# Kernel optimization log

Hardware: AMD Instinct MI355X
Metric: run time of the kernel (lower is better)

The kernel has to match this reference:

```python
import jax, jax.numpy as jnp
import numpy as np

B, S, D, H = 2, 2048, 1024, 16
DK = D // H  # 64
THETA = 10000.0


def setup_inputs() -> dict:
    key = jax.random.key(0)
    ks = jax.random.split(key, 5)
    std = float(np.sqrt(2.0 / (D + D)))
    x = jax.random.normal(ks[0], (B, S, D), dtype=jnp.float32)
    q_proj = jax.random.normal(ks[1], (D, D), dtype=jnp.float32) * std
    k_proj = jax.random.normal(ks[2], (D, D), dtype=jnp.float32) * std
    v_proj = jax.random.normal(ks[3], (D, D), dtype=jnp.float32) * std
    o_proj = jax.random.normal(ks[4], (D, D), dtype=jnp.float32) * std
    token_positions = jnp.arange(S, dtype=jnp.int32).reshape(1, S)
    return {"x": x, "token_positions": token_positions,
            "q_proj": q_proj, "k_proj": k_proj, "v_proj": v_proj, "o_proj": o_proj}


def _rope(t, pos):
    # t: [B, H, S, DK]; pos: [S]. Equivalent to multiplying by the block-diagonal
    # rotation matrix R[pos] in the source (interleaved 2x2 rotations).
    inv_freq = 1.0 / (THETA ** (2.0 * jnp.arange(DK // 2, dtype=jnp.float32) / DK))
    ang = pos.astype(jnp.float32)[:, None] * inv_freq[None, :]  # [S, DK/2]
    c, s = jnp.cos(ang), jnp.sin(ang)
    t0, t1 = t[..., 0::2], t[..., 1::2]
    out0 = c * t0 - s * t1
    out1 = s * t0 + c * t1
    return jnp.stack([out0, out1], axis=-1).reshape(t.shape)


def reference(x, token_positions, q_proj, k_proj, v_proj, o_proj):
    def split_heads(t):  # [B,S,D] -> [B,H,S,DK]
        return t.reshape(B, S, H, DK).transpose(0, 2, 1, 3)

    q = split_heads(jnp.einsum('bsd,ed->bse', x, q_proj))
    k = split_heads(jnp.einsum('bsd,ed->bse', x, k_proj))
    v = split_heads(jnp.einsum('bsd,ed->bse', x, v_proj))

    pos = token_positions[0]
    q = _rope(q, pos)
    k = _rope(k, pos)

    scores = jnp.einsum('bhqd,bhkd->bhqk', q, k) / jnp.sqrt(jnp.float32(DK))
    causal = jnp.tril(jnp.ones((S, S), dtype=bool))
    scores = jnp.where(causal, scores, -jnp.inf)

    # Faithful to source softmax: subtract the GLOBAL max (x.max()), then row-normalize.
    p = jnp.exp(scores - jnp.max(scores))
    p = p / jnp.sum(p, axis=-1, keepdims=True)

    attn = jnp.einsum('bhqk,bhkd->bhqd', p, v)
    attn = attn.transpose(0, 2, 1, 3).reshape(B, S, D)  # merge heads
    return jnp.einsum('bsd,ed->bse', attn, o_proj)
```

## Files before the change

### kernel.cpp

```cpp
#include <hip/hip_runtime.h>
#include <math.h>

#define B_  2
#define S_  2048
#define D_  1024
#define H_  16
#define DK_ 64
#define M_  (B_ * S_)

using u16 = unsigned short;
using u32 = unsigned int;
typedef __attribute__((ext_vector_type(8))) short  short8;
typedef __attribute__((ext_vector_type(4))) short  short4v;
typedef __attribute__((ext_vector_type(4))) float  float4v;
typedef __attribute__((ext_vector_type(4))) float  f32x4;
typedef __attribute__((ext_vector_type(4))) u32    u32x4;

__device__ __forceinline__ float bf2f(u16 h) {
  u32 u = ((u32)h) << 16;
  return __builtin_bit_cast(float, u);
}
__device__ __forceinline__ u16 f2bf(float f) {
  u32 u = __builtin_bit_cast(u32, f);
  u32 r = u + 0x7fffu + ((u >> 16) & 1u);
  return (u16)(r >> 16);
}

__device__ __forceinline__ void async16(const void* g, void* l) {
  __builtin_amdgcn_global_load_lds((const __attribute__((address_space(1))) void*)g,
                                   (__attribute__((address_space(3))) void*)l,
                                   16, 0, 0);
}

#define MFMA16(a, b, c) __builtin_amdgcn_mfma_f32_16x16x32_bf16((a), (b), (c), 0, 0, 0)

#define XG_  (M_ * D_ / 4)
#define WG_  (D_ * D_ / 4)
#define TOT_ (XG_ + 4 * WG_)
__global__ __launch_bounds__(256) void cvt5_kernel(
    const float* __restrict__ x,  const float* __restrict__ wq,
    const float* __restrict__ wk, const float* __restrict__ wv,
    const float* __restrict__ wo, u16* __restrict__ Xb, u16* __restrict__ Wqb,
    u16* __restrict__ Wkb, u16* __restrict__ Wvb, u16* __restrict__ Wob,
    float* __restrict__ tab, const void* __restrict__ posv) {
  int i = blockIdx.x * 256 + threadIdx.x;
  if (i >= TOT_) {
    const int j  = i - TOT_;
    const int s  = j >> 5, ii = j & 31;
    const int* p32 = (const int*)posv;
    const bool is64 = (p32[1] == 0 && p32[2] == 1);
    const int  ps   = is64 ? p32[2 * s] : p32[s];
    const float freq = exp2f(-0.4152410118609203f * (float)ii);
    float sn, cs;
    sincosf((float)ps * freq, &sn, &cs);
    tab[(size_t)j * 2]     = cs;
    tab[(size_t)j * 2 + 1] = sn;
    return;
  }
  const float* s; u16* d; int off;
  if (i < XG_)                { s = x;  d = Xb;  off = i; }
  else if (i < XG_ + WG_)     { s = wq; d = Wqb; off = i - XG_; }
  else if (i < XG_ + 2 * WG_) { s = wk; d = Wkb; off = i - XG_ - WG_; }
  else if (i < XG_ + 3 * WG_) { s = wv; d = Wvb; off = i - XG_ - 2 * WG_; }
  else                        { s = wo; d = Wob; off = i - XG_ - 3 * WG_; }
  f32x4 v = ((const f32x4*)s)[off];
  short4v o;
  o[0] = (short)f2bf(v[0]); o[1] = (short)f2bf(v[1]);
  o[2] = (short)f2bf(v[2]); o[3] = (short)f2bf(v[3]);
  ((short4v*)d)[off] = o;
}

template <int MODE, typename TC>
__device__ __forceinline__ void gemm_tile(const u16* __restrict__ A,
                                          const u16* __restrict__ Bw,
                                          TC* __restrict__ C,
                                          int K, int N, int m0, int n0,
                                          const float* __restrict__ tab,
                                          u16* __restrict__ As,
                                          u16* __restrict__ Bs) {
  const int tid  = threadIdx.x;
  const int lane = tid & 63;
  const int wave = tid >> 6;
  const int quad = lane >> 4;
  const int l15  = lane & 15;
  const int wm   = (wave >> 1) << 6;
  const int wn   = (wave & 1) << 6;

  float4v acc[4][4];
#pragma unroll
  for (int i = 0; i < 4; ++i)
#pragma unroll
    for (int j = 0; j < 4; ++j) acc[i][j] = (float4v){0.f, 0.f, 0.f, 0.f};

  for (int k0 = 0; k0 < K; k0 += 32) {
#pragma unroll
    for (int i = 0; i < 2; ++i) {
      const int cbase = i * 256 + wave * 64;
      const int c     = cbase + lane;
      async16(A  + (size_t)(m0 + (c >> 2)) * K + k0 + ((c & 3) << 3), As + cbase * 8);
      async16(Bw + (size_t)(n0 + (c >> 2)) * K + k0 + ((c & 3) << 3), Bs + cbase * 8);
    }
    __syncthreads();

    short8 af[4], bfr[4];
#pragma unroll
    for (int mi = 0; mi < 4; ++mi)
      af[mi] = *(const short8*)(As + (wm + mi * 16 + l15) * 32 + quad * 8);
#pragma unroll
    for (int ni = 0; ni < 4; ++ni)
      bfr[ni] = *(const short8*)(Bs + (wn + ni * 16 + l15) * 32 + quad * 8);
#pragma unroll
    for (int mi = 0; mi < 4; ++mi)
#pragma unroll
      for (int ni = 0; ni < 4; ++ni)
        acc[mi][ni] = MFMA16(af[mi], bfr[ni], acc[mi][ni]);
    __syncthreads();
  }

  if constexpr (MODE == 4) {
#pragma unroll
    for (int mi = 0; mi < 4; ++mi)
#pragma unroll
      for (int ni = 0; ni < 4; ++ni)
#pragma unroll
        for (int r = 0; r < 4; ++r) {
          const int row = m0 + wm + mi * 16 + quad * 4 + r;
          const int col = n0 + wn + ni * 16 + l15;
          C[(size_t)row * N + col] = acc[mi][ni][r];
        }
  } else if constexpr (MODE == 1 || MODE == 2) {
    const int p = l15 & 1;
#pragma unroll
    for (int mi = 0; mi < 4; ++mi)
#pragma unroll
      for (int r = 0; r < 4; ++r) {
        const int row = m0 + wm + mi * 16 + quad * 4 + r;
        const float* trow = tab + (size_t)(row & (S_ - 1)) * 64;
#pragma unroll
        for (int ni = 0; ni < 4; ++ni) {
          const int ii = ni * 8 + (l15 >> 1);
          const float cs = trow[2 * ii], sn = trow[2 * ii + 1];
          const float v  = acc[mi][ni][r];
          const float pr = __shfl_xor(v, 1, 64);
          const float t0 = p ? pr : v;
          const float t1 = p ? v : pr;
          float o = p ? (sn * t0 + cs * t1) : (cs * t0 - sn * t1);
          if constexpr (MODE == 1) o *= 0.125f;
          const int col = n0 + wn + ni * 16 + l15;
          ((u16*)C)[(size_t)row * N + col] = f2bf(o);
        }
      }
  } else {
#pragma unroll
    for (int ni = 0; ni < 4; ++ni) {
      const int col   = n0 + wn + ni * 16 + l15;
      const int sl    = col & (S_ - 1);
      const int wslot = ((l15 >> 2) << 3) + ((ni & 1) << 2) + (l15 & 3);
      const size_t cb = (size_t)(col >> 11) * ((size_t)D_ * S_) +
                        (size_t)((sl & ~31) + wslot);
#pragma unroll
      for (int mi = 0; mi < 4; ++mi)
#pragma unroll
        for (int r = 0; r < 4; ++r) {
          const int e = m0 + wm + mi * 16 + quad * 4 + r;
          ((u16*)C)[cb + (size_t)e * S_] = f2bf(acc[mi][ni][r]);
        }
    }
  }
}

__global__ __launch_bounds__(256) void gemm_qkv_kernel(
    const u16* __restrict__ X, const u16* __restrict__ Wq,
    const u16* __restrict__ Wk, const u16* __restrict__ Wv,
    u16* Qb, u16* Kb, u16* Vt, const float* __restrict__ tab) {
  __shared__ __align__(16) u16 As[128 * 32];
  __shared__ __align__(16) u16 Bs[128 * 32];
  const int bx  = blockIdx.x;
  const int nn  = blockIdx.y;
  const int sel = nn >> 3;
  if (sel == 0)
    gemm_tile<1>(X, Wq, Qb, D_, D_, bx * 128, (nn & 7) * 128, tab, As, Bs);
  else if (sel == 1)
    gemm_tile<2>(X, Wk, Kb, D_, D_, bx * 128, (nn & 7) * 128, tab, As, Bs);
  else
    gemm_tile<3>(Wv, X, Vt, D_, S_, (nn & 7) * 128, bx * 128, nullptr, As, Bs);
}

__global__ __launch_bounds__(256) void gemm_o_kernel(
    const u16* __restrict__ Ab, const u16* __restrict__ Wo, float* Out) {
  __shared__ __align__(16) u16 As[128 * 32];
  __shared__ __align__(16) u16 Bs[128 * 32];
  gemm_tile<4>(Ab, Wo, Out, D_, D_, blockIdx.x * 128, blockIdx.y * 128, nullptr,
               As, Bs);
}

__global__ __launch_bounds__(256, 4) void attn_kernel(const u16* __restrict__ Qb,
                                                      const u16* __restrict__ Kb,
                                                      const u16* __restrict__ Vt,
                                                      u16* __restrict__ Ob) {
  const int j5 = (blockIdx.x + blockIdx.y) & 31;
  const int r5 = j5 & 7, g5 = j5 >> 3;
  const int qt = (g5 == 0) ? r5 : (g5 == 1) ? r5 + 8 : (g5 == 2) ? 23 - r5 : 31 - r5;
  const int bh = blockIdx.y;
  const int b = bh >> 4, h = bh & 15;
  const int tid = threadIdx.x, lane = tid & 63, wave = tid >> 6;
  const int qh = wave >> 1, kh = wave & 1;
  const int quad = lane >> 4, l15 = lane & 15;
  const int qw = qt * 64 + qh * 32;

  __shared__ __align__(16) u16 SM[2][2][64 * 64];

  const char* kp = (const char*)(Kb + (size_t)b * S_ * D_ + h * DK_);
  const char* vp = (const char*)(Vt + (size_t)bh * DK_ * S_);

  int koffb[2], voffb[2];
#pragma unroll
  for (int i = 0; i < 2; ++i) {
    const int c  = wave * 128 + i * 64 + lane;
    const int kr = c >> 3;
    const int kj = (c & 7) ^ (kr & 7);
    koffb[i] = kr * (D_ * 2) + kj * 16;
    const int vdk = c >> 3;
    const int vj  = (c & 7) ^ (vdk & 7);
    voffb[i] = vdk * (S_ * 2) + vj * 16;
  }

  auto stage = [&](int sel) {
#pragma unroll
    for (int i = 0; i < 2; ++i) {
      const int cb = wave * 128 + i * 64;
      async16(kp + koffb[i], &SM[0][sel][cb * 8]);
      async16(vp + voffb[i], &SM[1][sel][cb * 8]);
    }
    kp += 64 * D_ * 2;
    vp += 128;
  };

  const int x7   = l15 & 7;
  const int krd0 = (kh * 32 + l15) * 64 + ((quad ^ x7) << 3);
  const int krd1 = (kh * 32 + l15) * 64 + (((quad + 4) ^ x7) << 3);
  const int vrd  = l15 * 64 + (((kh * 4 + quad) ^ x7) << 3);

  short8 qf[2][2];
#pragma unroll
  for (int rg = 0; rg < 2; ++rg) {
    const u16* qrow = Qb + (size_t)(b * S_ + qw + rg * 16 + l15) * D_ + h * DK_;
    qf[rg][0] = *(const short8*)(qrow + quad * 8);
    qf[rg][1] = *(const short8*)(qrow + 32 + quad * 8);
  }

  short8 ones;
#pragma unroll
  for (int j = 0; j < 8; ++j) ones[j] = (short)0x3F80;

  float4v oacc[2][4];
#pragma unroll
  for (int rg = 0; rg < 2; ++rg)
#pragma unroll
    for (int n2 = 0; n2 < 4; ++n2) oacc[rg][n2] = (float4v){0.f, 0.f, 0.f, 0.f};
  float4v lacc[2] = {(float4v){0.f, 0.f, 0.f, 0.f}, (float4v){0.f, 0.f, 0.f, 0.f}};

  const int NS = qt + 1;
  stage(0);

  for (int j = 0; j < NS; ++j) {
    asm volatile("s_waitcnt vmcnt(0)" ::: "memory");
    __builtin_amdgcn_s_barrier();
    asm volatile("" ::: "memory");
    if (j + 1 < NS) stage((j + 1) & 1);

    const u16* ks = &SM[0][j & 1][0];
    const u16* vs = &SM[1][j & 1][0];

    float4v sc[2][2];
    __builtin_amdgcn_s_setprio(1);
#pragma unroll
    for (int ni = 0; ni < 2; ++ni) {
      const short8 kf0 = *(const short8*)(ks + krd0 + ni * 1024);
      const short8 kf1 = *(const short8*)(ks + krd1 + ni * 1024);
      float4v z = (float4v){0.f, 0.f, 0.f, 0.f};
      sc[0][ni] = MFMA16(kf1, qf[0][1], MFMA16(kf0, qf[0][0], z));
      sc[1][ni] = MFMA16(kf1, qf[1][1], MFMA16(kf0, qf[1][0], z));
    }
    __builtin_amdgcn_s_setprio(0);

    const int kb = j * 64 + kh * 32;
    if (kb + 31 > qw) {
#pragma unroll
      for (int rg = 0; rg < 2; ++rg) {
        const int qr = qw + rg * 16 + l15;
#pragma unroll
        for (int ni = 0; ni < 2; ++ni)
#pragma unroll
          for (int r = 0; r < 4; ++r) {
            const float e = __expf(sc[rg][ni][r]);
            sc[rg][ni][r] = (kb + ni * 16 + quad * 4 + r > qr) ? 0.f : e;
          }
      }
    } else {
#pragma unroll
      for (int rg = 0; rg < 2; ++rg)
#pragma unroll
        for (int ni = 0; ni < 2; ++ni)
#pragma unroll
          for (int r = 0; r < 4; ++r) sc[rg][ni][r] = __expf(sc[rg][ni][r]);
    }

    short8 pfr[2];
#pragma unroll
    for (int rg = 0; rg < 2; ++rg) {
      u32 w0, w1, w2, w3;
      asm("v_cvt_pk_bf16_f32 %0, %1, %2" : "=v"(w0) : "v"(sc[rg][0][0]), "v"(sc[rg][0][1]));
      asm("v_cvt_pk_bf16_f32 %0, %1, %2" : "=v"(w1) : "v"(sc[rg][0][2]), "v"(sc[rg][0][3]));
      asm("v_cvt_pk_bf16_f32 %0, %1, %2" : "=v"(w2) : "v"(sc[rg][1][0]), "v"(sc[rg][1][1]));
      asm("v_cvt_pk_bf16_f32 %0, %1, %2" : "=v"(w3) : "v"(sc[rg][1][2]), "v"(sc[rg][1][3]));
      u32x4 ww = (u32x4){w0, w1, w2, w3};
      pfr[rg] = __builtin_bit_cast(short8, ww);
    }

    __builtin_amdgcn_s_setprio(1);
    lacc[0] = MFMA16(pfr[0], ones, lacc[0]);
    lacc[1] = MFMA16(pfr[1], ones, lacc[1]);
#pragma unroll
    for (int n2 = 0; n2 < 4; ++n2) {
      const short8 vf = *(const short8*)(vs + vrd + n2 * 1024);
      oacc[0][n2] = MFMA16(pfr[0], vf, oacc[0][n2]);
      oacc[1][n2] = MFMA16(pfr[1], vf, oacc[1][n2]);
    }
    __builtin_amdgcn_s_setprio(0);
  }

  __syncthreads();
  float* comb = (float*)(void*)&SM[0][0][0];
  if (kh == 1) {
    float* cw = comb + (size_t)(qh * 64 + lane) * 41;
#pragma unroll
    for (int rg = 0; rg < 2; ++rg) {
#pragma unroll
      for (int n2 = 0; n2 < 4; ++n2)
#pragma unroll
        for (int r = 0; r < 4; ++r) cw[rg * 16 + n2 * 4 + r] = oacc[rg][n2][r];
#pragma unroll
      for (int r = 0; r < 4; ++r) cw[32 + rg * 4 + r] = lacc[rg][r];
    }
  }
  __syncthreads();
  if (kh == 0) {
    const float* cw = comb + (size_t)(qh * 64 + lane) * 41;
#pragma unroll
    for (int rg = 0; rg < 2; ++rg) {
      float rinv[4];
#pragma unroll
      for (int r = 0; r < 4; ++r)
        rinv[r] = 1.0f / (lacc[rg][r] + cw[32 + rg * 4 + r]);
#pragma unroll
      for (int n2 = 0; n2 < 4; ++n2)
#pragma unroll
        for (int r = 0; r < 4; ++r) {
          const int srow = qw + rg * 16 + quad * 4 + r;
          Ob[(size_t)(b * S_ + srow) * D_ + h * DK_ + n2 * 16 + l15] =
              f2bf((oacc[rg][n2][r] + cw[rg * 16 + n2 * 4 + r]) * rinv[r]);
        }
    }
  }
}

extern "C" void kernel_launch(void* const* d_in, const int* in_sizes, int n_in,
                              void* d_out, int out_size, void* d_ws, size_t ws_size,
                              hipStream_t stream) {
  const float* x  = (const float*)d_in[0];
  const void*  tp = d_in[1];
  const float* wq = (const float*)d_in[2];
  const float* wk = (const float*)d_in[3];
  const float* wv = (const float*)d_in[4];
  const float* wo = (const float*)d_in[5];
  float* out = (float*)d_out;

  u16* Qb  = (u16*)d_ws;
  u16* Kb  = Qb + (size_t)M_ * D_;
  u16* Vt  = Kb + (size_t)M_ * D_;
  u16* Ab  = Vt + (size_t)M_ * D_;
  u16* Xb  = Ab;
  u16* Wqb = Ab + (size_t)M_ * D_;
  u16* Wkb = Wqb + (size_t)D_ * D_;
  u16* Wvb = Wkb + (size_t)D_ * D_;
  u16* Wob = Wvb + (size_t)D_ * D_;
  float* tab = (float*)(Wob + (size_t)D_ * D_);

  cvt5_kernel<<<dim3((TOT_ + 65536) / 256), dim3(256), 0, stream>>>(
      x, wq, wk, wv, wo, Xb, Wqb, Wkb, Wvb, Wob, tab, tp);
  gemm_qkv_kernel<<<dim3(32, 24), dim3(256), 0, stream>>>(Xb, Wqb, Wkb, Wvb,
                                                          Qb, Kb, Vt, tab);
  attn_kernel<<<dim3(32, 32), dim3(256), 0, stream>>>(Qb, Kb, Vt, Ab);
  gemm_o_kernel<<<dim3(32, 8), dim3(256), 0, stream>>>(Ab, Wob, out);
}
```

Baseline: 185.1 us.

## Triple-buffer GEMM LDS tiles with async prefetch two stages ahead

Replaces the load-sync-compute-sync loop in the shared GEMM tile routine with a three-stage ring of LDS buffers. Global-to-LDS async copies for step t+2 are issued while step t is computed, synchronised with explicit vmcnt waits and a single barrier per iteration. The aim is to hide global memory latency behind the MFMA work in the QKV and output projection GEMMs. It triples LDS use per block (48 KB) and depends on the vmcnt counts matching the number of outstanding async loads.

After: 193.6 us. 1.05x slower.

```diff
diff --git a/kernel.cpp b/kernel.cpp
--- a/kernel.cpp
+++ b/kernel.cpp
@@ -86,35 +86,63 @@
   const int wm   = (wave >> 1) << 6;
   const int wn   = (wave & 1) << 6;
 
+  int aoff[2], boff[2], lb[2];
+#pragma unroll
+  for (int i = 0; i < 2; ++i) {
+    const int cbase = i * 256 + wave * 64;
+    const int c     = cbase + lane;
+    aoff[i] = (m0 + (c >> 2)) * K + ((c & 3) << 3);
+    boff[i] = (n0 + (c >> 2)) * K + ((c & 3) << 3);
+    lb[i]   = cbase * 8;
+  }
+
+  auto stage = [&](int t, int buf) {
+    const int k0 = t << 5;
+    u16* as = As + buf * 4096;
+    u16* bs = Bs + buf * 4096;
+#pragma unroll
+    for (int i = 0; i < 2; ++i) {
+      async16(A  + (size_t)(aoff[i] + k0), as + lb[i]);
+      async16(Bw + (size_t)(boff[i] + k0), bs + lb[i]);
+    }
+  };
+
   float4v acc[4][4];
 #pragma unroll
   for (int i = 0; i < 4; ++i)
 #pragma unroll
     for (int j = 0; j < 4; ++j) acc[i][j] = (float4v){0.f, 0.f, 0.f, 0.f};
 
-  for (int k0 = 0; k0 < K; k0 += 32) {
-#pragma unroll
-    for (int i = 0; i < 2; ++i) {
-      const int cbase = i * 256 + wave * 64;
-      const int c     = cbase + lane;
-      async16(A  + (size_t)(m0 + (c >> 2)) * K + k0 + ((c & 3) << 3), As + cbase * 8);
-      async16(Bw + (size_t)(n0 + (c >> 2)) * K + k0 + ((c & 3) << 3), Bs + cbase * 8);
-    }
-    __syncthreads();
+  const int NT = K >> 5;
+  stage(0, 0);
+  stage(1, 1);
+  int cbuf = 0, sbuf = 2;
+
+  for (int t = 0; t < NT; ++t) {
+    if (t + 1 < NT) { asm volatile("s_waitcnt vmcnt(4)" ::: "memory"); }
+    else            { asm volatile("s_waitcnt vmcnt(0)" ::: "memory"); }
+    __builtin_amdgcn_s_barrier();
+    asm volatile("" ::: "memory");
+    if (t + 2 < NT) {
+      stage(t + 2, sbuf);
+      sbuf = (sbuf == 2) ? 0 : sbuf + 1;
+    }
+    const u16* as = As + cbuf * 4096;
+    const u16* bs = Bs + cbuf * 4096;
+    cbuf = (cbuf == 2) ? 0 : cbuf + 1;
 
     short8 af[4], bfr[4];
 #pragma unroll
     for (int mi = 0; mi < 4; ++mi)
-      af[mi] = *(const short8*)(As + (wm + mi * 16 + l15) * 32 + quad * 8);
+      af[mi] = *(const short8*)(as + (wm + mi * 16 + l15) * 32 + quad * 8);
 #pragma unroll
     for (int ni = 0; ni < 4; ++ni)
-      bfr[ni] = *(const short8*)(Bs + (wn + ni * 16 + l15) * 32 + quad * 8);
+      bfr[ni] = *(const short8*)(bs + (wn + ni * 16 + l15) * 32 + quad * 8);
 #pragma unroll
     for (int mi = 0; mi < 4; ++mi)
 #pragma unroll
       for (int ni = 0; ni < 4; ++ni)
         acc[mi][ni] = MFMA16(af[mi], bfr[ni], acc[mi][ni]);
-    __syncthreads();
   }
 
   if constexpr (MODE == 4) {
@@ -173,8 +201,8 @@
     const u16* __restrict__ X, const u16* __restrict__ Wq,
     const u16* __restrict__ Wk, const u16* __restrict__ Wv,
     u16* Qb, u16* Kb, u16* Vt, const float* __restrict__ tab) {
-  __shared__ __align__(16) u16 As[128 * 32];
-  __shared__ __align__(16) u16 Bs[128 * 32];
+  __shared__ __align__(16) u16 As[3 * 128 * 32];
+  __shared__ __align__(16) u16 Bs[3 * 128 * 32];
   const int bx  = blockIdx.x;
   const int nn  = blockIdx.y;
   const int sel = nn >> 3;
@@ -188,8 +216,8 @@
 
 __global__ __launch_bounds__(256) void gemm_o_kernel(
     const u16* __restrict__ Ab, const u16* __restrict__ Wo, float* Out) {
-  __shared__ __align__(16) u16 As[128 * 32];
-  __shared__ __align__(16) u16 Bs[128 * 32];
+  __shared__ __align__(16) u16 As[3 * 128 * 32];
+  __shared__ __align__(16) u16 Bs[3 * 128 * 32];
   gemm_tile<4>(Ab, Wo, Out, D_, D_, blockIdx.x * 128, blockIdx.y * 128, nullptr,
                As, Bs);
 }
```

## Double GEMM K-step to 64, XOR-swizzle LDS, bounce V-transpose stores through LDS

Applied to the files above, without the earlier changes.

The shared GEMM tile now loads a 64-wide K slice per iteration with an XOR-swizzled LDS layout, and precomputes the global and LDS offsets once. This halves the number of barrier pairs and is meant to cut LDS bank conflicts. The V-projection epilogue, which wrote the transposed output as scattered 2-byte stores, now stages the tile in LDS and writes 16-byte coalesced rows. LDS per block grows to 32 KB, which may reduce occupancy.

Result: no change. 185.3 us (+0.1%).

```diff
diff --git a/kernel.cpp b/kernel.cpp
--- a/kernel.cpp
+++ b/kernel.cpp
@@ -76,8 +76,9 @@
                                           TC* __restrict__ C,
                                           int K, int N, int m0, int n0,
                                           const float* __restrict__ tab,
-                                          u16* __restrict__ As,
-                                          u16* __restrict__ Bs) {
+                                          u16* __restrict__ SMEM) {
+  u16* As = SMEM;
+  u16* Bs = SMEM + 128 * 64;
   const int tid  = threadIdx.x;
   const int lane = tid & 63;
   const int wave = tid >> 6;
@@ -86,34 +87,52 @@
   const int wm   = (wave >> 1) << 6;
   const int wn   = (wave & 1) << 6;
 
+  int aoff[4], boff[4], lb[4];
+#pragma unroll
+  for (int i = 0; i < 4; ++i) {
+    const int cb  = wave * 256 + i * 64;
+    const int c   = cb + lane;
+    const int row = c >> 3;
+    const int gch = (c & 7) ^ (row & 7);
+    aoff[i] = (m0 + row) * K + gch * 8;
+    boff[i] = (n0 + row) * K + gch * 8;
+    lb[i]   = cb * 8;
+  }
+
+  const int x7 = l15 & 7;
+  int ard[2];
+#pragma unroll
+  for (int kk = 0; kk < 2; ++kk)
+    ard[kk] = l15 * 64 + ((((kk << 2) + quad) ^ x7) << 3);
+
   float4v acc[4][4];
 #pragma unroll
   for (int i = 0; i < 4; ++i)
 #pragma unroll
     for (int j = 0; j < 4; ++j) acc[i][j] = (float4v){0.f, 0.f, 0.f, 0.f};
 
-  for (int k0 = 0; k0 < K; k0 += 32) {
-#pragma unroll
-    for (int i = 0; i < 2; ++i) {
-      const int cbase = i * 256 + wave * 64;
-      const int c     = cbase + lane;
-      async16(A  + (size_t)(m0 + (c >> 2)) * K + k0 + ((c & 3) << 3), As + cbase * 8);
-      async16(Bw + (size_t)(n0 + (c >> 2)) * K + k0 + ((c & 3) << 3), Bs + cbase * 8);
+  for (int k0 = 0; k0 < K; k0 += 64) {
+#pragma unroll
+    for (int i = 0; i < 4; ++i) {
+      async16(A  + (size_t)(aoff[i] + k0), As + lb[i]);
+      async16(Bw + (size_t)(boff[i] + k0), Bs + lb[i]);
     }
     __syncthreads();
-
-    short8 af[4], bfr[4];
-#pragma unroll
-    for (int mi = 0; mi < 4; ++mi)
-      af[mi] = *(const short8*)(As + (wm + mi * 16 + l15) * 32 + quad * 8);
-#pragma unroll
-    for (int ni = 0; ni < 4; ++ni)
-      bfr[ni] = *(const short8*)(Bs + (wn + ni * 16 + l15) * 32 + quad * 8);
-#pragma unroll
-    for (int mi = 0; mi < 4; ++mi)
+#pragma unroll
+    for (int kk = 0; kk < 2; ++kk) {
+      short8 af[4], bfr[4];
+#pragma unroll
+      for (int mi = 0; mi < 4; ++mi)
+        af[mi] = *(const short8*)(As + (wm + mi * 16) * 64 + ard[kk]);
 #pragma unroll
       for (int ni = 0; ni < 4; ++ni)
-        acc[mi][ni] = MFMA16(af[mi], bfr[ni], acc[mi][ni]);
+        bfr[ni] = *(const short8*)(Bs + (wn + ni * 16) * 64 + ard[kk]);
+#pragma unroll
+      for (int mi = 0; mi < 4; ++mi)
+#pragma unroll
+        for (int ni = 0; ni < 4; ++ni)
+          acc[mi][ni] = MFMA16(af[mi], bfr[ni], acc[mi][ni]);
+    }
     __syncthreads();
   }
 
@@ -151,20 +170,32 @@
         }
       }
   } else {
+    u16* bounce = SMEM;
 #pragma unroll
     for (int ni = 0; ni < 4; ++ni) {
-      const int col   = n0 + wn + ni * 16 + l15;
-      const int sl    = col & (S_ - 1);
+      const int cl    = wn + ni * 16 + l15;
       const int wslot = ((l15 >> 2) << 3) + ((ni & 1) << 2) + (l15 & 3);
-      const size_t cb = (size_t)(col >> 11) * ((size_t)D_ * S_) +
-                        (size_t)((sl & ~31) + wslot);
+      const int cp    = (cl & ~31) | wslot;
 #pragma unroll
       for (int mi = 0; mi < 4; ++mi)
 #pragma unroll
         for (int r = 0; r < 4; ++r) {
-          const int e = m0 + wm + mi * 16 + quad * 4 + r;
-          ((u16*)C)[cb + (size_t)e * S_] = f2bf(acc[mi][ni][r]);
+          const int e = wm + mi * 16 + quad * 4 + r;
+          bounce[e * 128 + (cp ^ ((e & 7) << 3))] = f2bf(acc[mi][ni][r]);
         }
+    }
+    __syncthreads();
+    const int e  = tid >> 1;
+    const int hf = (tid & 1) << 6;
+    const size_t b   = (size_t)(n0 >> 11);
+    const int    sl0 = n0 & (S_ - 1);
+    u16* dst = (u16*)C + b * ((size_t)D_ * S_) + (size_t)(m0 + e) * S_ + sl0 + hf;
+    const u16* srcb = bounce + e * 128;
+    const int  ck   = e & 7;
+#pragma unroll
+    for (int i2 = 0; i2 < 8; ++i2) {
+      const int sc = (((hf >> 3) + i2) ^ ck) << 3;
+      *(short8*)(dst + i2 * 8) = *(const short8*)(srcb + sc);
     }
   }
 }
@@ -173,25 +204,23 @@
     const u16* __restrict__ X, const u16* __restrict__ Wq,
     const u16* __restrict__ Wk, const u16* __restrict__ Wv,
     u16* Qb, u16* Kb, u16* Vt, const float* __restrict__ tab) {
-  __shared__ __align__(16) u16 As[128 * 32];
-  __shared__ __align__(16) u16 Bs[128 * 32];
+  __shared__ __align__(16) u16 SMEM[128 * 128];
   const int bx  = blockIdx.x;
   const int nn  = blockIdx.y;
   const int sel = nn >> 3;
   if (sel == 0)
-    gemm_tile<1>(X, Wq, Qb, D_, D_, bx * 128, (nn & 7) * 128, tab, As, Bs);
+    gemm_tile<1>(X, Wq, Qb, D_, D_, bx * 128, (nn & 7) * 128, tab, SMEM);
   else if (sel == 1)
-    gemm_tile<2>(X, Wk, Kb, D_, D_, bx * 128, (nn & 7) * 128, tab, As, Bs);
+    gemm_tile<2>(X, Wk, Kb, D_, D_, bx * 128, (nn & 7) * 128, tab, SMEM);
   else
-    gemm_tile<3>(Wv, X, Vt, D_, S_, (nn & 7) * 128, bx * 128, nullptr, As, Bs);
+    gemm_tile<3>(Wv, X, Vt, D_, S_, (nn & 7) * 128, bx * 128, nullptr, SMEM);
 }
 
 __global__ __launch_bounds__(256) void gemm_o_kernel(
     const u16* __restrict__ Ab, const u16* __restrict__ Wo, float* Out) {
-  __shared__ __align__(16) u16 As[128 * 32];
-  __shared__ __align__(16) u16 Bs[128 * 32];
+  __shared__ __align__(16) u16 SMEM[128 * 128];
   gemm_tile<4>(Ab, Wo, Out, D_, D_, blockIdx.x * 128, blockIdx.y * 128, nullptr,
-               As, Bs);
+               SMEM);
 }
 
 __global__ __launch_bounds__(256, 4) void attn_kernel(const u16* __restrict__ Qb,
```
